# Performance work log

Hardware: AMD Instinct MI355X
Metric: run time of the kernel (lower is better)

## Reference

```python
import jax, jax.numpy as jnp
import numpy as np
from jax.ops import segment_sum

N_NODES = 100000
N_EDGES = 1600000
N_GRAPHS = 128
HIDDEN = 128
N_CLASSES = 10


def setup_inputs() -> dict:
    key = jax.random.key(0)
    ks = jax.random.split(key, 8)
    src = jax.random.randint(ks[0], (N_EDGES,), 0, N_NODES, dtype=jnp.int32)
    dst = jax.random.randint(ks[1], (N_EDGES,), 0, N_NODES, dtype=jnp.int32)
    graph_ids = jnp.sort(jax.random.randint(ks[2], (N_NODES,), 0, N_GRAPHS, dtype=jnp.int32))
    W1 = jax.random.normal(ks[3], (1, HIDDEN), dtype=jnp.float32)
    b1 = jnp.zeros((HIDDEN,), jnp.float32)
    W2 = jax.random.normal(ks[4], (HIDDEN, HIDDEN), dtype=jnp.float32) * 0.05
    b2 = jnp.zeros((HIDDEN,), jnp.float32)
    Wc = jax.random.normal(ks[5], (HIDDEN, N_CLASSES), dtype=jnp.float32) * 0.05
    bc = jnp.zeros((N_CLASSES,), jnp.float32)
    return {"src": src, "dst": dst, "graph_ids": graph_ids,
            "W1": W1, "b1": b1, "W2": W2, "b2": b2, "Wc": Wc, "bc": bc}


def _graph_conv(h, src, dst, norm_src, norm_dst, W, b, n_nodes):
    # DGL GraphConv, norm='both': D_out^{-1/2} gather -> scatter-sum -> W -> D_in^{-1/2} -> +b
    hs = h * norm_src[:, None]
    agg = segment_sum(hs[src], dst, num_segments=n_nodes)  # [N, F_in]
    return agg @ W * norm_dst[:, None] + b


def reference(src, dst, graph_ids, W1, b1, W2, b2, Wc, bc):
    n_nodes = graph_ids.shape[0]
    ones_e = jnp.ones(src.shape[0], jnp.float32)
    indeg = segment_sum(ones_e, dst, num_segments=n_nodes)
    outdeg = segment_sum(ones_e, src, num_segments=n_nodes)
    norm_src = jnp.clip(outdeg, 1.0, None) ** -0.5
    norm_dst = jnp.clip(indeg, 1.0, None) ** -0.5

    h = indeg[:, None]  # node feature = in-degree, [N, 1]
    h = jax.nn.relu(_graph_conv(h, src, dst, norm_src, norm_dst, W1, b1, n_nodes))
    h = jax.nn.relu(_graph_conv(h, src, dst, norm_src, norm_dst, W2, b2, n_nodes))

    # dgl.mean_nodes: per-graph mean pooling
    sums = segment_sum(h, graph_ids, num_segments=N_GRAPHS)          # [G, H]
    cnts = segment_sum(jnp.ones(n_nodes, jnp.float32), graph_ids, num_segments=N_GRAPHS)
    hg = sums / jnp.clip(cnts, 1.0, None)[:, None]
    return hg @ Wc + bc  # [G, n_classes]
```

## Files before the change

### kernel.cpp

```cpp
#include <hip/hip_runtime.h>

#define N_NODES   100000
#define N_EDGES   1600000
#define N_GRAPHS  128
#define HIDDEN    128
#define N_CLASSES 10

#define BSH   9
#define BSZ   512
#define NBUCK 196
#define CAP   16384
#define PCH   4096
#define PTH   512
#define PIT   (PCH / PTH)

typedef unsigned int   uint;
typedef unsigned short ushort;
typedef unsigned char  uchar;

__global__ __launch_bounds__(PTH)
void k_part(const int* __restrict__ src, const int* __restrict__ dst,
            unsigned* __restrict__ bcur1, unsigned* __restrict__ bcur2,
            unsigned* __restrict__ tmp1, ushort* __restrict__ tmp2, int nE) {
    __shared__ unsigned hist[256], scanT[256], lcur[256], base[256];
    __shared__ unsigned stag4[PCH];
    __shared__ uchar    stagB[PCH];
    int t = threadIdx.x;
    int e0 = blockIdx.x * PCH;
    int e1 = min(e0 + PCH, nE);
    int cntE = e1 - e0;

    int sv[PIT], dv[PIT];
    if (t < 256) hist[t] = 0;
    __syncthreads();
    #pragma unroll
    for (int m = 0; m < PIT; ++m) {
        int e = e0 + t + m * PTH;
        if (e < e1) {
            sv[m] = src[e]; dv[m] = dst[e];
            atomicAdd(&hist[dv[m] >> BSH], 1u);
        }
    }
    __syncthreads();
    unsigned v = (t < 256) ? hist[t] : 0u;
    if (t < 256) scanT[t] = v;
    __syncthreads();
    for (int off = 1; off < 256; off <<= 1) {
        unsigned add = (t < 256 && t >= off) ? scanT[t - off] : 0u;
        __syncthreads();
        if (t < 256) scanT[t] += add;
        __syncthreads();
    }
    if (t < 256) {
        unsigned excl = scanT[t] - v;
        lcur[t] = excl;
        if (v > 0) { unsigned g = atomicAdd(&bcur1[t], v); base[t] = (unsigned)t * CAP + g - excl; }
    }
    __syncthreads();
    #pragma unroll
    for (int m = 0; m < PIT; ++m) {
        int e = e0 + t + m * PTH;
        if (e < e1) {
            int d = dv[m], s = sv[m];
            int b = d >> BSH;
            unsigned p = atomicAdd(&lcur[b], 1u);
            stag4[p] = ((unsigned)(d & (BSZ - 1)) << 17) | (unsigned)s;
            stagB[p] = (uchar)b;
        }
    }
    __syncthreads();
    for (int i = t; i < cntE; i += PTH) {
        unsigned b = stagB[i];
        unsigned a = base[b] + (unsigned)i;
        if (a < (b + 1u) * CAP) tmp1[a] = stag4[i];
    }
    __syncthreads();

    if (t < 256) hist[t] = 0;
    __syncthreads();
    #pragma unroll
    for (int m = 0; m < PIT; ++m) {
        int e = e0 + t + m * PTH;
        if (e < e1) atomicAdd(&hist[sv[m] >> BSH], 1u);
    }
    __syncthreads();
    v = (t < 256) ? hist[t] : 0u;
    if (t < 256) scanT[t] = v;
    __syncthreads();
    for (int off = 1; off < 256; off <<= 1) {
        unsigned add = (t < 256 && t >= off) ? scanT[t - off] : 0u;
        __syncthreads();
        if (t < 256) scanT[t] += add;
        __syncthreads();
    }
    if (t < 256) {
        unsigned excl = scanT[t] - v;
        lcur[t] = excl;
        if (v > 0) { unsigned g = atomicAdd(&bcur2[t], v); base[t] = (unsigned)t * CAP + g - excl; }
    }
    __syncthreads();
    #pragma unroll
    for (int m = 0; m < PIT; ++m) {
        int e = e0 + t + m * PTH;
        if (e < e1) {
            int s = sv[m];
            unsigned p = atomicAdd(&lcur[s >> BSH], 1u);
            stag4[p] = (unsigned)s;
        }
    }
    __syncthreads();
    for (int i = t; i < cntE; i += PTH) {
        unsigned s = stag4[i];
        unsigned b = s >> BSH;
        unsigned a = base[b] + (unsigned)i;
        if (a < (b + 1u) * CAP) tmp2[a] = (ushort)(s & (BSZ - 1));
    }
}

__global__ __launch_bounds__(1024)
void k_cnt(const unsigned* __restrict__ bcur1, const unsigned* __restrict__ tmp1,
           const unsigned* __restrict__ bcur2, const ushort* __restrict__ tmp2,
           float* __restrict__ ns, float* __restrict__ hs0, float* __restrict__ ndv) {
    __shared__ unsigned cin[BSZ], cout[BSZ];
    int b = blockIdx.x, t = threadIdx.x;
    if (t < BSZ) { cin[t] = 0; cout[t] = 0; }
    __syncthreads();
    unsigned f1 = min(bcur1[b], (unsigned)CAP);
    const unsigned* tp1 = tmp1 + (size_t)b * CAP;
    for (unsigned i = t; i < f1; i += 1024) atomicAdd(&cin[tp1[i] >> 17], 1u);
    unsigned f2 = min(bcur2[b], (unsigned)CAP);
    const ushort* tp2 = tmp2 + (size_t)b * CAP;
    for (unsigned i = t; i < f2; i += 1024) atomicAdd(&cout[tp2[i]], 1u);
    __syncthreads();
    if (t < BSZ) {
        int n = b * BSZ + t;
        if (n < N_NODES) {
            unsigned ci = cin[t];
            float nsv = rsqrtf(fmaxf((float)cout[t], 1.0f));
            ns[n]  = nsv;
            hs0[n] = (float)ci * nsv;
            ndv[n] = rsqrtf(fmaxf((float)ci, 1.0f));
        }
    }
}

__global__ __launch_bounds__(512)
void k_info(const unsigned* __restrict__ bcur1, const unsigned* __restrict__ tmp1,
            const float* __restrict__ hs0, const float* __restrict__ ns,
            const float* __restrict__ ndv,
            const float* __restrict__ W1, const float* __restrict__ b1,
            const float* __restrict__ W2,
            float* __restrict__ U, float* __restrict__ V,
            float4* __restrict__ info) {
    __shared__ float agg[BSZ];
    __shared__ float stu[128];
    __shared__ float sts[128];
    int b = blockIdx.x, t = threadIdx.x;
    agg[t] = 0.0f;
    if (t < 128) {
        float w = W1[t], bb = b1[t];
        stu[t] = (w != 0.0f) ? (-bb / w) : 1e30f;
    }
    __syncthreads();
    if (b < 129) {
        if (t < 128) sts[t] = stu[t];
        __syncthreads();
        for (int k = 2; k <= 128; k <<= 1) {
            for (int j = k >> 1; j > 0; j >>= 1) {
                if (t < 128) {
                    int ixj = t ^ j;
                    if (ixj > t) {
                        float a = sts[t], bb = sts[ixj];
                        bool up = ((t & k) == 0);
                        if (up ? (a > bb) : (a < bb)) { sts[t] = bb; sts[ixj] = a; }
                    }
                }
                __syncthreads();
            }
        }
        if (t < 128) {
            int sg = b;
            float a_rep;
            if (sg == 0)        a_rep = sts[0]   - 1.0f;
            else if (sg == 128) a_rep = sts[127] + 1.0f;
            else                a_rep = 0.5f * (sts[sg - 1] + sts[sg]);
            float u = 0.0f, vv = 0.0f;
            #pragma unroll 8
            for (int j = 0; j < 128; ++j) {
                float w  = W1[j], bb = b1[j];
                float w2 = W2[j * HIDDEN + t];
                bool on  = (a_rep * w + bb > 0.0f);
                u  += on ? w  * w2 : 0.0f;
                vv += on ? bb * w2 : 0.0f;
            }
            U[sg * HIDDEN + t] = u;
            V[sg * HIDDEN + t] = vv;
        }
    }
    unsigned f1 = min(bcur1[b], (unsigned)CAP);
    const unsigned* tp1 = tmp1 + (size_t)b * CAP;
    for (unsigned i = t; i < f1; i += 512) {
        unsigned e = tp1[i];
        atomicAdd(&agg[e >> 17], hs0[e & 0x1FFFFu]);
    }
    __syncthreads();
    int n = b * BSZ + t;
    if (n < N_NODES) {
        float nd = ndv[n];
        float av = agg[t] * nd;
        int sgp = 0;
        #pragma unroll 16
        for (int q = 0; q < 128; ++q) sgp += (stu[q] < av) ? 1 : 0;
        float nsv = ns[n];
        info[n] = make_float4(nsv * av, nsv, __int_as_float(sgp), nd);
    }
}

__global__ __launch_bounds__(512)
void k_conv2(const unsigned* __restrict__ bcur1, const unsigned* __restrict__ tmp1,
             const float4* __restrict__ info,
             const float* __restrict__ U, const float* __restrict__ V,
             const int* __restrict__ graph_ids, const float* __restrict__ b2,
             float* __restrict__ pool, float* __restrict__ cnt) {
    __shared__ float aggA[BSZ], aggB[BSZ];
    __shared__ uint  smn[BSZ], smx[BSZ];
    int b = blockIdx.x, t = threadIdx.x;
    aggA[t] = 0.0f; aggB[t] = 0.0f; smn[t] = 255u; smx[t] = 0u;
    __syncthreads();
    unsigned f1 = min(bcur1[b], (unsigned)CAP);
    const unsigned* tp1 = tmp1 + (size_t)b * CAP;
    for (unsigned i = t; i < f1; i += 512) {
        unsigned e = tp1[i];
        unsigned dl = e >> 17;
        float4 nf = info[e & 0x1FFFFu];
        atomicAdd(&aggA[dl], nf.x);
        atomicAdd(&aggB[dl], nf.y);
        uint sg = (uint)__float_as_int(nf.z);
        atomicMin(&smn[dl], sg);
        atomicMax(&smx[dl], sg);
    }
    __syncthreads();

    int d = t & 127, q = t >> 7;
    float bbd = b2[d];
    int base = b * BSZ;
    int nmax = min(BSZ, N_NODES - base);
    int gcur = -1; float racc = 0.0f, cl = 0.0f;
    for (int i = q; i < nmax; i += 4) {
        int n = base + i;
        uint mn = smn[i], mx = smx[i];
        float acc;
        if (mn >= mx) {
            uint sg = min(mn, 128u);
            acc = aggA[i] * U[sg * HIDDEN + d] + aggB[i] * V[sg * HIDDEN + d];
        } else {
            acc = 0.0f;
            for (unsigned k = 0; k < f1; ++k) {
                unsigned e = tp1[k];
                if ((e >> 17) == (unsigned)i) {
                    float4 nf = info[e & 0x1FFFFu];
                    uint sg = (uint)__float_as_int(nf.z);
                    acc += nf.x * U[sg * HIDDEN + d] + nf.y * V[sg * HIDDEN + d];
                }
            }
        }
        float nd = info[n].w;
        float row = fmaxf(nd * acc + bbd, 0.0f);
        int g = graph_ids[n];
        if (g != gcur) {
            if (gcur >= 0) {
                atomicAdd(&pool[gcur * HIDDEN + d], racc);
                if (d == 0) atomicAdd(&cnt[gcur], cl);
            }
            gcur = g; racc = 0.0f; cl = 0.0f;
        }
        racc += row; cl += 1.0f;
    }
    if (gcur >= 0) {
        atomicAdd(&pool[gcur * HIDDEN + d], racc);
        if (d == 0) atomicAdd(&cnt[gcur], cl);
    }
}

__global__ void k_final(const float* __restrict__ pool, const float* __restrict__ cnt,
                        const float* __restrict__ Wc, const float* __restrict__ bc,
                        float* __restrict__ out) {
    int t = blockIdx.x * blockDim.x + threadIdx.x;
    if (t >= N_GRAPHS * N_CLASSES) return;
    int g = t / N_CLASSES, c = t % N_CLASSES;
    float inv = 1.0f / fmaxf(cnt[g], 1.0f);
    float acc = bc[c];
    for (int j = 0; j < HIDDEN; ++j)
        acc += pool[g * HIDDEN + j] * inv * Wc[j * N_CLASSES + c];
    out[t] = acc;
}

extern "C" void kernel_launch(void* const* d_in, const int* in_sizes, int n_in,
                              void* d_out, int out_size, void* d_ws, size_t ws_size,
                              hipStream_t stream) {
    const int*   src       = (const int*)d_in[0];
    const int*   dst       = (const int*)d_in[1];
    const int*   graph_ids = (const int*)d_in[2];
    const float* W1        = (const float*)d_in[3];
    const float* b1        = (const float*)d_in[4];
    const float* W2        = (const float*)d_in[5];
    const float* b2        = (const float*)d_in[6];
    const float* Wc        = (const float*)d_in[7];
    const float* bc        = (const float*)d_in[8];
    float* out = (float*)d_out;

    char* ws = (char*)d_ws;
    size_t off = 0;
    auto alloc = [&](size_t elems) { void* p = ws + off; off += elems * 4; return p; };

    unsigned* bcur1 = (unsigned*)alloc(256);
    unsigned* bcur2 = (unsigned*)alloc(256);
    float*    pool  = (float*)   alloc(N_GRAPHS * HIDDEN);
    float*    cnt   = (float*)   alloc(N_GRAPHS);
    size_t zero_bytes = off;
    float4*   info  = (float4*)  alloc((size_t)N_NODES * 4);
    unsigned* tmp1  = (unsigned*)alloc((size_t)NBUCK * CAP);
    ushort*   tmp2  = (ushort*)  alloc((size_t)NBUCK * CAP / 2);
    float*    nsA   = (float*)   alloc(N_NODES);
    float*    hs0   = (float*)   alloc(N_NODES);
    float*    ndv   = (float*)   alloc(N_NODES);
    float*    U     = (float*)   alloc(129 * HIDDEN);
    float*    V     = (float*)   alloc(129 * HIDDEN);

    hipMemsetAsync(d_ws, 0, zero_bytes, stream);

    int pblocks = (N_EDGES + PCH - 1) / PCH;
    k_part <<<pblocks, PTH, 0, stream>>>(src, dst, bcur1, bcur2, tmp1, tmp2, N_EDGES);
    k_cnt  <<<NBUCK, 1024, 0, stream>>>(bcur1, tmp1, bcur2, tmp2, nsA, hs0, ndv);
    k_info <<<NBUCK, 512, 0, stream>>>(bcur1, tmp1, hs0, nsA, ndv, W1, b1, W2, U, V, info);
    k_conv2<<<NBUCK, 512, 0, stream>>>(bcur1, tmp1, info, U, V, graph_ids, b2, pool, cnt);
    k_final<<<(N_GRAPHS * N_CLASSES + 255) / 256, 256, 0, stream>>>(pool, cnt, Wc, bc, out);
}
```

Measured before the change: 190.3 us.

## Halve bucket size to 256 nodes, widen blocks to 1024, use wave-shuffle scan

Node buckets shrink from 512 to 256 nodes, so there are 391 buckets instead of 196 and more blocks keep the GPU's compute units busy. The per-chunk histogram scan now uses wavefront shuffles across 512 bins instead of a barrier-heavy shared-memory scan. The edge loops in the count, info and conv2 kernels run 1024 threads and are unrolled four-way to keep more gathers in flight. Risks include more partition bins with fewer elements each, and more threads per node-row loop in conv2 (stride 8) over less shared data.

```diff
diff --git a/kernel.cpp b/kernel.cpp
--- a/kernel.cpp
+++ b/kernel.cpp
@@ -6,32 +6,51 @@
 #define HIDDEN    128
 #define N_CLASSES 10
 
-#define BSH   9
-#define BSZ   512
-#define NBUCK 196
-#define CAP   16384
+#define BSH   8
+#define BSZ   256
+#define NBUCK 391
+#define NBIN  512
+#define CAP   8192
 #define PCH   4096
 #define PTH   512
 #define PIT   (PCH / PTH)
 
 typedef unsigned int   uint;
 typedef unsigned short ushort;
-typedef unsigned char  uchar;
+
+__device__ __forceinline__ uint scan_excl_512(uint v, int t, uint* wtmp) {
+    uint lane = (uint)(t & 63);
+    uint incl = v;
+    #pragma unroll
+    for (int off = 1; off < 64; off <<= 1) {
+        uint up = __shfl_up(incl, off, 64);
+        if (lane >= (uint)off) incl += up;
+    }
+    if (lane == 63) wtmp[t >> 6] = incl;
+    __syncthreads();
+    uint wo = 0;
+    int w = t >> 6;
+    #pragma unroll
+    for (int k = 0; k < 7; ++k) wo += (k < w) ? wtmp[k] : 0u;
+    __syncthreads();
+    return incl + wo - v;
+}
 
 __global__ __launch_bounds__(PTH)
 void k_part(const int* __restrict__ src, const int* __restrict__ dst,
-            unsigned* __restrict__ bcur1, unsigned* __restrict__ bcur2,
-            unsigned* __restrict__ tmp1, ushort* __restrict__ tmp2, int nE) {
-    __shared__ unsigned hist[256], scanT[256], lcur[256], base[256];
-    __shared__ unsigned stag4[PCH];
-    __shared__ uchar    stagB[PCH];
+            uint* __restrict__ bcur1, uint* __restrict__ bcur2,
+            uint* __restrict__ tmp1, ushort* __restrict__ tmp2, int nE) {
+    __shared__ uint   hist[NBIN], lcur[NBIN], base[NBIN];
+    __shared__ uint   wtmp[8];
+    __shared__ uint   stag4[PCH];
+    __shared__ ushort stagB[PCH];
     int t = threadIdx.x;
     int e0 = blockIdx.x * PCH;
     int e1 = min(e0 + PCH, nE);
     int cntE = e1 - e0;
 
     int sv[PIT], dv[PIT];
-    if (t < 256) hist[t] = 0;
+    hist[t] = 0;
     __syncthreads();
     #pragma unroll
     for (int m = 0; m < PIT; ++m) {
@@ -42,20 +61,10 @@
         }
     }
     __syncthreads();
-    unsigned v = (t < 256) ? hist[t] : 0u;
-    if (t < 256) scanT[t] = v;
-    __syncthreads();
-    for (int off = 1; off < 256; off <<= 1) {
-        unsigned add = (t < 256 && t >= off) ? scanT[t - off] : 0u;
-        __syncthreads();
-        if (t < 256) scanT[t] += add;
-        __syncthreads();
-    }
-    if (t < 256) {
-        unsigned excl = scanT[t] - v;
-        lcur[t] = excl;
-        if (v > 0) { unsigned g = atomicAdd(&bcur1[t], v); base[t] = (unsigned)t * CAP + g - excl; }
-    }
+    uint v = hist[t];
+    uint excl = scan_excl_512(v, t, wtmp);
+    lcur[t] = excl;
+    if (v > 0) { uint g = atomicAdd(&bcur1[t], v); base[t] = (uint)t * CAP + g - excl; }
     __syncthreads();
     #pragma unroll
     for (int m = 0; m < PIT; ++m) {
@@ -63,20 +72,20 @@
         if (e < e1) {
             int d = dv[m], s = sv[m];
             int b = d >> BSH;
-            unsigned p = atomicAdd(&lcur[b], 1u);
-            stag4[p] = ((unsigned)(d & (BSZ - 1)) << 17) | (unsigned)s;
-            stagB[p] = (uchar)b;
+            uint p = atomicAdd(&lcur[b], 1u);
+            stag4[p] = ((uint)(d & (BSZ - 1)) << 17) | (uint)s;
+            stagB[p] = (ushort)b;
         }
     }
     __syncthreads();
     for (int i = t; i < cntE; i += PTH) {
-        unsigned b = stagB[i];
-        unsigned a = base[b] + (unsigned)i;
+        uint b = stagB[i];
+        uint a = base[b] + (uint)i;
         if (a < (b + 1u) * CAP) tmp1[a] = stag4[i];
     }
     __syncthreads();
 
-    if (t < 256) hist[t] = 0;
+    hist[t] = 0;
     __syncthreads();
     #pragma unroll
     for (int m = 0; m < PIT; ++m) {
@@ -84,58 +93,60 @@
         if (e < e1) atomicAdd(&hist[sv[m] >> BSH], 1u);
     }
     __syncthreads();
-    v = (t < 256) ? hist[t] : 0u;
-    if (t < 256) scanT[t] = v;
-    __syncthreads();
-    for (int off = 1; off < 256; off <<= 1) {
-        unsigned add = (t < 256 && t >= off) ? scanT[t - off] : 0u;
-        __syncthreads();
-        if (t < 256) scanT[t] += add;
-        __syncthreads();
-    }
-    if (t < 256) {
-        unsigned excl = scanT[t] - v;
-        lcur[t] = excl;
-        if (v > 0) { unsigned g = atomicAdd(&bcur2[t], v); base[t] = (unsigned)t * CAP + g - excl; }
-    }
+    v = hist[t];
+    excl = scan_excl_512(v, t, wtmp);
+    lcur[t] = excl;
+    if (v > 0) { uint g = atomicAdd(&bcur2[t], v); base[t] = (uint)t * CAP + g - excl; }
     __syncthreads();
     #pragma unroll
     for (int m = 0; m < PIT; ++m) {
         int e = e0 + t + m * PTH;
         if (e < e1) {
             int s = sv[m];
-            unsigned p = atomicAdd(&lcur[s >> BSH], 1u);
-            stag4[p] = (unsigned)s;
+            uint p = atomicAdd(&lcur[s >> BSH], 1u);
+            stag4[p] = (uint)s;
         }
     }
     __syncthreads();
     for (int i = t; i < cntE; i += PTH) {
-        unsigned s = stag4[i];
-        unsigned b = s >> BSH;
-        unsigned a = base[b] + (unsigned)i;
+        uint s = stag4[i];
+        uint b = s >> BSH;
+        uint a = base[b] + (uint)i;
         if (a < (b + 1u) * CAP) tmp2[a] = (ushort)(s & (BSZ - 1));
     }
 }
 
 __global__ __launch_bounds__(1024)
-void k_cnt(const unsigned* __restrict__ bcur1, const unsigned* __restrict__ tmp1,
-           const unsigned* __restrict__ bcur2, const ushort* __restrict__ tmp2,
+void k_cnt(const uint* __restrict__ bcur1, const uint* __restrict__ tmp1,
+           const uint* __restrict__ bcur2, const ushort* __restrict__ tmp2,
            float* __restrict__ ns, float* __restrict__ hs0, float* __restrict__ ndv) {
-    __shared__ unsigned cin[BSZ], cout[BSZ];
+    __shared__ uint cin[BSZ], cout[BSZ];
     int b = blockIdx.x, t = threadIdx.x;
     if (t < BSZ) { cin[t] = 0; cout[t] = 0; }
     __syncthreads();
-    unsigned f1 = min(bcur1[b], (unsigned)CAP);
-    const unsigned* tp1 = tmp1 + (size_t)b * CAP;
-    for (unsigned i = t; i < f1; i += 1024) atomicAdd(&cin[tp1[i] >> 17], 1u);
-    unsigned f2 = min(bcur2[b], (unsigned)CAP);
+    uint f1 = min(bcur1[b], (uint)CAP);
+    const uint* tp1 = tmp1 + (size_t)b * CAP;
+    uint i = t;
+    for (; i + 3072u < f1; i += 4096u) {
+        uint a0 = tp1[i], a1 = tp1[i + 1024], a2 = tp1[i + 2048], a3 = tp1[i + 3072];
+        atomicAdd(&cin[a0 >> 17], 1u); atomicAdd(&cin[a1 >> 17], 1u);
+        atomicAdd(&cin[a2 >> 17], 1u); atomicAdd(&cin[a3 >> 17], 1u);
+    }
+    for (; i < f1; i += 1024u) atomicAdd(&cin[tp1[i] >> 17], 1u);
+    uint f2 = min(bcur2[b], (uint)CAP);
     const ushort* tp2 = tmp2 + (size_t)b * CAP;
-    for (unsigned i = t; i < f2; i += 1024) atomicAdd(&cout[tp2[i]], 1u);
+    i = t;
+    for (; i + 3072u < f2; i += 4096u) {
+        uint a0 = tp2[i], a1 = tp2[i + 1024], a2 = tp2[i + 2048], a3 = tp2[i + 3072];
+        atomicAdd(&cout[a0], 1u); atomicAdd(&cout[a1], 1u);
+        atomicAdd(&cout[a2], 1u); atomicAdd(&cout[a3], 1u);
+    }
+    for (; i < f2; i += 1024u) atomicAdd(&cout[tp2[i]], 1u);
     __syncthreads();
     if (t < BSZ) {
         int n = b * BSZ + t;
         if (n < N_NODES) {
-            unsigned ci = cin[t];
+            uint ci = cin[t];
             float nsv = rsqrtf(fmaxf((float)cout[t], 1.0f));
             ns[n]  = nsv;
             hs0[n] = (float)ci * nsv;
@@ -144,8 +155,8 @@
     }
 }
 
-__global__ __launch_bounds__(512)
-void k_info(const unsigned* __restrict__ bcur1, const unsigned* __restrict__ tmp1,
+__global__ __launch_bounds__(1024)
+void k_info(const uint* __restrict__ bcur1, const uint* __restrict__ tmp1,
             const float* __restrict__ hs0, const float* __restrict__ ns,
             const float* __restrict__ ndv,
             const float* __restrict__ W1, const float* __restrict__ b1,
@@ -156,7 +167,7 @@
     __shared__ float stu[128];
     __shared__ float sts[128];
     int b = blockIdx.x, t = threadIdx.x;
-    agg[t] = 0.0f;
+    if (t < BSZ) agg[t] = 0.0f;
     if (t < 128) {
         float w = W1[t], bb = b1[t];
         stu[t] = (w != 0.0f) ? (-bb / w) : 1e30f;
@@ -197,15 +208,23 @@
             V[sg * HIDDEN + t] = vv;
         }
     }
-    unsigned f1 = min(bcur1[b], (unsigned)CAP);
-    const unsigned* tp1 = tmp1 + (size_t)b * CAP;
-    for (unsigned i = t; i < f1; i += 512) {
-        unsigned e = tp1[i];
+    uint f1 = min(bcur1[b], (uint)CAP);
+    const uint* tp1 = tmp1 + (size_t)b * CAP;
+    uint i = t;
+    for (; i + 3072u < f1; i += 4096u) {
+        uint e0 = tp1[i], e1 = tp1[i + 1024], e2 = tp1[i + 2048], e3 = tp1[i + 3072];
+        float h0 = hs0[e0 & 0x1FFFFu], h1 = hs0[e1 & 0x1FFFFu];
+        float h2 = hs0[e2 & 0x1FFFFu], h3 = hs0[e3 & 0x1FFFFu];
+        atomicAdd(&agg[e0 >> 17], h0); atomicAdd(&agg[e1 >> 17], h1);
+        atomicAdd(&agg[e2 >> 17], h2); atomicAdd(&agg[e3 >> 17], h3);
+    }
+    for (; i < f1; i += 1024u) {
+        uint e = tp1[i];
         atomicAdd(&agg[e >> 17], hs0[e & 0x1FFFFu]);
     }
     __syncthreads();
     int n = b * BSZ + t;
-    if (n < N_NODES) {
+    if (t < BSZ && n < N_NODES) {
         float nd = ndv[n];
         float av = agg[t] * nd;
         int sgp = 0;
@@ -216,22 +235,41 @@
     }
 }
 
-__global__ __launch_bounds__(512)
-void k_conv2(const unsigned* __restrict__ bcur1, const unsigned* __restrict__ tmp1,
-             const float4* __restrict__ info,
+__global__ __launch_bounds__(1024)
+void k_conv2(const uint* __restrict__ bcur1, const uint* __restrict__ tmp1,
+             const float4* __restrict__ info, const float* __restrict__ ndv,
              const float* __restrict__ U, const float* __restrict__ V,
              const int* __restrict__ graph_ids, const float* __restrict__ b2,
              float* __restrict__ pool, float* __restrict__ cnt) {
     __shared__ float aggA[BSZ], aggB[BSZ];
     __shared__ uint  smn[BSZ], smx[BSZ];
     int b = blockIdx.x, t = threadIdx.x;
-    aggA[t] = 0.0f; aggB[t] = 0.0f; smn[t] = 255u; smx[t] = 0u;
-    __syncthreads();
-    unsigned f1 = min(bcur1[b], (unsigned)CAP);
-    const unsigned* tp1 = tmp1 + (size_t)b * CAP;
-    for (unsigned i = t; i < f1; i += 512) {
-        unsigned e = tp1[i];
-        unsigned dl = e >> 17;
+    if (t < BSZ) { aggA[t] = 0.0f; aggB[t] = 0.0f; smn[t] = 255u; smx[t] = 0u; }
+    __syncthreads();
+    uint f1 = min(bcur1[b], (uint)CAP);
+    const uint* tp1 = tmp1 + (size_t)b * CAP;
+    uint i = t;
+    for (; i + 3072u < f1; i += 4096u) {
+        uint e0 = tp1[i], e1 = tp1[i + 1024], e2 = tp1[i + 2048], e3 = tp1[i + 3072];
+        float4 n0 = info[e0 & 0x1FFFFu];
+        float4 n1 = info[e1 & 0x1FFFFu];
+        float4 n2 = info[e2 & 0x1FFFFu];
+        float4 n3 = info[e3 & 0x1FFFFu];
+        uint d0 = e0 >> 17, d1 = e1 >> 17, d2 = e2 >> 17, d3 = e3 >> 17;
+        atomicAdd(&aggA[d0], n0.x); atomicAdd(&aggB[d0], n0.y);
+        atomicAdd(&aggA[d1], n1.x); atomicAdd(&aggB[d1], n1.y);
+        atomicAdd(&aggA[d2], n2.x); atomicAdd(&aggB[d2], n2.y);
+        atomicAdd(&aggA[d3], n3.x); atomicAdd(&aggB[d3], n3.y);
+        uint s0 = (uint)__float_as_int(n0.z), s1 = (uint)__float_as_int(n1.z);
+        uint s2 = (uint)__float_as_int(n2.z), s3 = (uint)__float_as_int(n3.z);
+        atomicMin(&smn[d0], s0); atomicMax(&smx[d0], s0);
+        atomicMin(&smn[d1], s1); atomicMax(&smx[d1], s1);
+        atomicMin(&smn[d2], s2); atomicMax(&smx[d2], s2);
+        atomicMin(&smn[d3], s3); atomicMax(&smx[d3], s3);
+    }
+    for (; i < f1; i += 1024u) {
+        uint e = tp1[i];
+        uint dl = e >> 17;
         float4 nf = info[e & 0x1FFFFu];
         atomicAdd(&aggA[dl], nf.x);
         atomicAdd(&aggB[dl], nf.y);
@@ -246,25 +284,25 @@
     int base = b * BSZ;
     int nmax = min(BSZ, N_NODES - base);
     int gcur = -1; float racc = 0.0f, cl = 0.0f;
-    for (int i = q; i < nmax; i += 4) {
-        int n = base + i;
-        uint mn = smn[i], mx = smx[i];
+    for (int r = q; r < nmax; r += 8) {
+        int n = base + r;
+        uint mn = smn[r], mx = smx[r];
         float acc;
         if (mn >= mx) {
             uint sg = min(mn, 128u);
-            acc = aggA[i] * U[sg * HIDDEN + d] + aggB[i] * V[sg * HIDDEN + d];
+            acc = aggA[r] * U[sg * HIDDEN + d] + aggB[r] * V[sg * HIDDEN + d];
         } else {
             acc = 0.0f;
-            for (unsigned k = 0; k < f1; ++k) {
-                unsigned e = tp1[k];
-                if ((e >> 17) == (unsigned)i) {
+            for (uint k = 0; k < f1; ++k) {
+                uint e = tp1[k];
+                if ((e >> 17) == (uint)r) {
                     float4 nf = info[e & 0x1FFFFu];
                     uint sg = (uint)__float_as_int(nf.z);
                     acc += nf.x * U[sg * HIDDEN + d] + nf.y * V[sg * HIDDEN + d];
                 }
             }
         }
-        float nd = info[n].w;
+        float nd = ndv[n];
         float row = fmaxf(nd * acc + bbd, 0.0f);
         int g = graph_ids[n];
         if (g != gcur) {
@@ -313,26 +351,26 @@
     size_t off = 0;
     auto alloc = [&](size_t elems) { void* p = ws + off; off += elems * 4; return p; };
 
-    unsigned* bcur1 = (unsigned*)alloc(256);
-    unsigned* bcur2 = (unsigned*)alloc(256);
-    float*    pool  = (float*)   alloc(N_GRAPHS * HIDDEN);
-    float*    cnt   = (float*)   alloc(N_GRAPHS);
+    uint*  bcur1 = (uint*) alloc(NBIN);
+    uint*  bcur2 = (uint*) alloc(NBIN);
+    float* pool  = (float*)alloc(N_GRAPHS * HIDDEN);
+    float* cnt   = (float*)alloc(N_GRAPHS);
     size_t zero_bytes = off;
-    float4*   info  = (float4*)  alloc((size_t)N_NODES * 4);
-    unsigned* tmp1  = (unsigned*)alloc((size_t)NBUCK * CAP);
-    ushort*   tmp2  = (ushort*)  alloc((size_t)NBUCK * CAP / 2);
-    float*    nsA   = (float*)   alloc(N_NODES);
-    float*    hs0   = (float*)   alloc(N_NODES);
-    float*    ndv   = (float*)   alloc(N_NODES);
-    float*    U     = (float*)   alloc(129 * HIDDEN);
-    float*    V     = (float*)   alloc(129 * HIDDEN);
+    float4* info = (float4*)alloc((size_t)N_NODES * 4);
+    uint*   tmp1 = (uint*)  alloc((size_t)NBUCK * CAP);
+    ushort* tmp2 = (ushort*)alloc((size_t)NBUCK * CAP / 2);
+    float*  nsA  = (float*) alloc(N_NODES);
+    float*  hs0  = (float*) alloc(N_NODES);
+    float*  ndv  = (float*) alloc(N_NODES);
+    float*  U    = (float*) alloc(129 * HIDDEN);
+    float*  V    = (float*) alloc(129 * HIDDEN);
 
     hipMemsetAsync(d_ws, 0, zero_bytes, stream);
 
     int pblocks = (N_EDGES + PCH - 1) / PCH;
     k_part <<<pblocks, PTH, 0, stream>>>(src, dst, bcur1, bcur2, tmp1, tmp2, N_EDGES);
     k_cnt  <<<NBUCK, 1024, 0, stream>>>(bcur1, tmp1, bcur2, tmp2, nsA, hs0, ndv);
-    k_info <<<NBUCK, 512, 0, stream>>>(bcur1, tmp1, hs0, nsA, ndv, W1, b1, W2, U, V, info);
-    k_conv2<<<NBUCK, 512, 0, stream>>>(bcur1, tmp1, info, U, V, graph_ids, b2, pool, cnt);
+    k_info <<<NBUCK, 1024, 0, stream>>>(bcur1, tmp1, hs0, nsA, ndv, W1, b1, W2, U, V, info);
+    k_conv2<<<NBUCK, 1024, 0, stream>>>(bcur1, tmp1, info, ndv, U, V, graph_ids, b2, pool, cnt);
     k_final<<<(N_GRAPHS * N_CLASSES + 255) / 256, 256, 0, stream>>>(pool, cnt, Wc, bc, out);
 }
```

Result: faster. 175.0 us (-8.1%).
